# Optimization experiments

Hardware: AMD Instinct MI355X
Metric: run time of the kernel (lower is better)

The kernel has to match this reference:

```python
import jax, jax.numpy as jnp
import numpy as np

FP8_MAX = 448.0  # max representable magnitude of float8_e4m3fn


def _quantize_tensorwise(x):
    """Tensor-wise fp8 quantization. Returns (fp8 tensor, inverse_scale) where
    dequant = fp8.astype(f32) * inverse_scale (matches Fp8Quantization.quantize_tensorwise)."""
    amax = jnp.max(jnp.abs(x))
    inv_scale = jnp.maximum(amax / FP8_MAX, jnp.float32(1e-12))
    q = (x / inv_scale).astype(jnp.float8_e4m3fn)
    return q, inv_scale


def _fp8_mm(qa, qb, sa, sb):
    # scaled fp8 GEMM: accumulate in f32, apply product of per-tensor inverse scales
    return (qa.astype(jnp.float32) @ qb.astype(jnp.float32)) * (sa * sb)


def setup_inputs() -> dict:
    key = jax.random.key(0)
    k1, k2, k3 = jax.random.split(key, 3)
    x = jax.random.normal(k1, (4, 2048, 2048), dtype=jnp.float32)
    weight = jax.random.normal(k2, (2048, 2048), dtype=jnp.float32) * 0.02
    bias = jax.random.normal(k3, (2048,), dtype=jnp.float32) * 0.01
    return {"x": x, "weight": weight, "bias": bias}


def reference(x, weight, bias):
    # flatten leading dims: inputmat = input.view(-1, K)
    K = x.shape[-1]
    xm = x.reshape(-1, K)                      # [T, K]
    qx, sx = _quantize_tensorwise(xm)          # fp8 input + inverse scale
    qwt, swt = _quantize_tensorwise(weight.T)  # fp8 weight^T [K, N] + inverse scale
    out = _fp8_mm(qx, qwt, sx, swt) + bias     # [T, N]
    return out.reshape(*x.shape[:-1], -1)
```

## Files before the change

### kernel.cpp

```cpp
#include <hip/hip_runtime.h>
#include <stdint.h>

typedef float f32x4 __attribute__((ext_vector_type(4)));
typedef int   i32x4 __attribute__((ext_vector_type(4)));
typedef int   i32x8 __attribute__((ext_vector_type(8)));

__global__ __launch_bounds__(256) void amax2_kernel(
    const float* __restrict__ x, int nx4,
    const float* __restrict__ w, int nw4,
    int xblocks, int* __restrict__ out) {
  const float4* src;
  int n4, j0, stride, slot;
  if ((int)blockIdx.x < xblocks) {
    src = (const float4*)x; n4 = nx4; slot = 0;
    j0 = blockIdx.x * blockDim.x + threadIdx.x;
    stride = xblocks * blockDim.x;
  } else {
    src = (const float4*)w; n4 = nw4; slot = 1;
    j0 = (blockIdx.x - xblocks) * blockDim.x + threadIdx.x;
    stride = (gridDim.x - xblocks) * blockDim.x;
  }
  float m = 0.f;
  for (int j = j0; j < n4; j += stride) {
    float4 v = src[j];
    m = fmaxf(m, fmaxf(fmaxf(fabsf(v.x), fabsf(v.y)),
                       fmaxf(fabsf(v.z), fabsf(v.w))));
  }
#pragma unroll
  for (int off = 32; off; off >>= 1)
    m = fmaxf(m, __shfl_down(m, off, 64));
  __shared__ float red[4];
  const int lane = threadIdx.x & 63;
  const int wv = threadIdx.x >> 6;
  if (lane == 0) red[wv] = m;
  __syncthreads();
  if (threadIdx.x == 0) {
    m = fmaxf(fmaxf(red[0], red[1]), fmaxf(red[2], red[3]));
    atomicMax(out + slot, (int)__float_as_uint(m));
  }
}

__global__ __launch_bounds__(256) void quant2_kernel(
    const float* __restrict__ x, unsigned char* __restrict__ qx, int nx4,
    const float* __restrict__ w, unsigned char* __restrict__ qw, int nw4,
    int xblocks, const unsigned* __restrict__ amax2) {
  const float4* src;
  unsigned* dst;
  int n4, j0, stride;
  float amax;
  if ((int)blockIdx.x < xblocks) {
    src = (const float4*)x; dst = (unsigned*)qx; n4 = nx4;
    amax = __uint_as_float(amax2[0]);
    j0 = blockIdx.x * blockDim.x + threadIdx.x;
    stride = xblocks * blockDim.x;
  } else {
    src = (const float4*)w; dst = (unsigned*)qw; n4 = nw4;
    amax = __uint_as_float(amax2[1]);
    j0 = (blockIdx.x - xblocks) * blockDim.x + threadIdx.x;
    stride = (gridDim.x - xblocks) * blockDim.x;
  }
  const float inv_scale = fmaxf(amax / 448.0f, 1e-12f);
  for (int j = j0; j < n4; j += stride) {
    float4 v = src[j];
    float a0 = v.x / inv_scale;
    float a1 = v.y / inv_scale;
    float a2 = v.z / inv_scale;
    float a3 = v.w / inv_scale;
    int p = 0;
    p = __builtin_amdgcn_cvt_pk_fp8_f32(a0, a1, p, false);
    p = __builtin_amdgcn_cvt_pk_fp8_f32(a2, a3, p, true);
    dst[j] = (unsigned)p;
  }
}

#define BM 256
#define BN 256
#define BK 128
#define GEMM_LDS_BYTES (4 * 32768)

__device__ __forceinline__ void load_lds16(const void* g, void* l) {
  __builtin_amdgcn_global_load_lds(
      (const __attribute__((address_space(1))) unsigned int*)g,
      (__attribute__((address_space(3))) unsigned int*)l, 16, 0, 0);
}

__global__ __launch_bounds__(512, 2) void gemm_fp8_kernel(
    const unsigned char* __restrict__ Aq,
    const unsigned char* __restrict__ Bq,
    const float* __restrict__ bias,
    const unsigned* __restrict__ amax2,
    float* __restrict__ out,
    int T, int N, int K) {
  extern __shared__ unsigned char smem[];
  unsigned char* sA = smem;
  unsigned char* sB = smem + 65536;

  const int tid  = threadIdx.x;
  const int lane = tid & 63;
  const int wave = tid >> 6;
  const int wm = (wave >> 2) * 128;
  const int wn = (wave & 3) * 64;

  int lin = (int)(blockIdx.y * gridDim.x + blockIdx.x);
  const int nwg = (int)(gridDim.x * gridDim.y);
  if ((nwg & 7) == 0) lin = (lin & 7) * (nwg >> 3) + (lin >> 3);
  const long m0 = (long)(lin / (int)gridDim.x) * BM;
  const long n0 = (long)(lin % (int)gridDim.x) * BN;

  const long Kl = (long)K;

  const int row_s = tid >> 3;
  const int scol  = ((tid & 7) ^ (row_s & 7)) << 4;
  const int t16   = tid << 4;

  const int lm = lane & 15;
  const int qh = lane >> 4;
  const int c0 = ((qh * 2)     ^ (lm & 7)) << 4;
  const int c1 = ((qh * 2 + 1) ^ (lm & 7)) << 4;

  auto STAGE_A = [&](int Ts) {
    const unsigned char* g = Aq + (m0 + row_s) * Kl + (long)Ts * BK + scol;
    unsigned char* l = sA + ((Ts & 1) << 15) + t16;
    load_lds16(g, l);
    load_lds16(g +  64 * Kl, l + 8192);
    load_lds16(g + 128 * Kl, l + 16384);
    load_lds16(g + 192 * Kl, l + 24576);
  };
  auto STAGE_B = [&](int Ts) {
    const unsigned char* g = Bq + (n0 + row_s) * Kl + (long)Ts * BK + scol;
    unsigned char* l = sB + ((Ts & 1) << 15) + t16;
    load_lds16(g, l);
    load_lds16(g +  64 * Kl, l + 8192);
    load_lds16(g + 128 * Kl, l + 16384);
    load_lds16(g + 192 * Kl, l + 24576);
  };
  auto LDA = [&](const unsigned char* base, int mt) {
    const unsigned char* p = base + (wm + mt * 16 + lm) * BK;
    i32x4 lo = *(const i32x4*)(p + c0);
    i32x4 hi = *(const i32x4*)(p + c1);
    return (i32x8){lo.x, lo.y, lo.z, lo.w, hi.x, hi.y, hi.z, hi.w};
  };
  auto LDB = [&](const unsigned char* base, int nt) {
    const unsigned char* p = base + (wn + nt * 16 + lm) * BK;
    i32x4 lo = *(const i32x4*)(p + c0);
    i32x4 hi = *(const i32x4*)(p + c1);
    return (i32x8){lo.x, lo.y, lo.z, lo.w, hi.x, hi.y, hi.z, hi.w};
  };

  f32x4 acc[8][4];
#pragma unroll
  for (int i = 0; i < 8; ++i)
#pragma unroll
    for (int j = 0; j < 4; ++j) acc[i][j] = (f32x4){0.f, 0.f, 0.f, 0.f};

  const int nt = K / BK;

  STAGE_A(0); STAGE_B(0);
  asm volatile("s_waitcnt vmcnt(0)" ::: "memory");
  __builtin_amdgcn_s_barrier();
  __builtin_amdgcn_sched_barrier(0);

#define MFMA(ai, bj, ci)                                                 \
  acc[ci][bj] = __builtin_amdgcn_mfma_scale_f32_16x16x128_f8f6f4(        \
      af[ai], bf[bj], acc[ci][bj], 0, 0, 0, 0x7f7f7f7f, 0, 0x7f7f7f7f)

  i32x8 af[4], bf[4];
  for (int t = 0; t < nt; ++t) {
    const unsigned char* a = sA + ((t & 1) << 15);
    const unsigned char* b = sB + ((t & 1) << 15);

    if (t + 1 < nt) { STAGE_A(t + 1); STAGE_B(t + 1); }

    af[0] = LDA(a, 0); af[1] = LDA(a, 1); af[2] = LDA(a, 2); af[3] = LDA(a, 3);
    bf[0] = LDB(b, 0); bf[1] = LDB(b, 1); bf[2] = LDB(b, 2); bf[3] = LDB(b, 3);
#pragma unroll
    for (int i = 0; i < 4; ++i) {
      MFMA(i, 0, i); MFMA(i, 1, i); MFMA(i, 2, i); MFMA(i, 3, i);
    }

    __builtin_amdgcn_sched_barrier(0);

    af[0] = LDA(a, 4); af[1] = LDA(a, 5); af[2] = LDA(a, 6); af[3] = LDA(a, 7);
#pragma unroll
    for (int i = 0; i < 4; ++i) {
      MFMA(i, 0, 4 + i); MFMA(i, 1, 4 + i); MFMA(i, 2, 4 + i); MFMA(i, 3, 4 + i);
    }

    asm volatile("s_waitcnt vmcnt(0)" ::: "memory");
    __builtin_amdgcn_s_barrier();
    __builtin_amdgcn_sched_barrier(0);
  }
#undef MFMA

  const float fsx = fmaxf(__uint_as_float(amax2[0]) / 448.0f, 1e-12f);
  const float fsw = fmaxf(__uint_as_float(amax2[1]) / 448.0f, 1e-12f);
  const float scale = fsx * fsw;
  const int rbase = qh * 4;
  float bv[4];
#pragma unroll
  for (int j = 0; j < 4; ++j) bv[j] = bias[n0 + wn + j * 16 + lm];
#pragma unroll
  for (int mt = 0; mt < 8; ++mt) {
#pragma unroll
    for (int r = 0; r < 4; ++r) {
      const long row = m0 + wm + mt * 16 + rbase + r;
      float* orow = out + row * (long)N + n0 + wn;
#pragma unroll
      for (int j = 0; j < 4; ++j)
        orow[j * 16 + lm] = acc[mt][j][r] * scale + bv[j];
    }
  }
}

extern "C" void kernel_launch(void* const* d_in, const int* in_sizes, int n_in,
                              void* d_out, int out_size, void* d_ws, size_t ws_size,
                              hipStream_t stream) {
  const float* x = (const float*)d_in[0];
  const float* w = (const float*)d_in[1];
  const float* bias = (const float*)d_in[2];
  float* out = (float*)d_out;

  const int N = in_sizes[2];
  const int K = in_sizes[1] / N;
  const int T = in_sizes[0] / K;

  unsigned* amax2 = (unsigned*)d_ws;
  unsigned char* qx = (unsigned char*)d_ws + 256;
  unsigned char* qw = qx + (size_t)T * K;

  const int XB = 1024;
  const int WB = 256;
  amax2_kernel<<<XB + WB, 256, 0, stream>>>(x, T * K / 4, w, N * K / 4, XB,
                                            (int*)amax2);
  quant2_kernel<<<XB + WB, 256, 0, stream>>>(x, qx, T * K / 4, w, qw, N * K / 4,
                                             XB, amax2);

  static bool lds_attr_set = false;
  if (!lds_attr_set) {
    (void)hipFuncSetAttribute((const void*)gemm_fp8_kernel,
                              hipFuncAttributeMaxDynamicSharedMemorySize,
                              GEMM_LDS_BYTES);
    lds_attr_set = true;
  }
  dim3 grid(N / BN, T / BM);
  gemm_fp8_kernel<<<grid, 512, GEMM_LDS_BYTES, stream>>>(qx, qw, bias, amax2,
                                                         out, T, N, K);
}
```

Before: 178.7 us.

## Use 4 waves with 128x128 warp tiles in fp8 GEMM

The GEMM workgroup shrinks from 8 waves to 4, and each wave now computes a 128x128 output tile (8x8 MFMA tiles) instead of 128x64. Each thread issues twice as many global-to-LDS loads per stage, and all A and B fragments are loaded before one 64-MFMA block. The aim is more register-level reuse per LDS read and fewer waves contending for LDS. The cost is 256 accumulator registers per thread plus fragments, which risks spills or low occupancy, and less overlap between LDS reads and MFMAs.

```diff
diff --git a/kernel.cpp b/kernel.cpp
--- a/kernel.cpp
+++ b/kernel.cpp
@@ -84,7 +84,7 @@
       (__attribute__((address_space(3))) unsigned int*)l, 16, 0, 0);
 }
 
-__global__ __launch_bounds__(512, 2) void gemm_fp8_kernel(
+__global__ __launch_bounds__(256, 1) void gemm_fp8_kernel(
     const unsigned char* __restrict__ Aq,
     const unsigned char* __restrict__ Bq,
     const float* __restrict__ bias,
@@ -98,8 +98,8 @@
   const int tid  = threadIdx.x;
   const int lane = tid & 63;
   const int wave = tid >> 6;
-  const int wm = (wave >> 2) * 128;
-  const int wn = (wave & 3) * 64;
+  const int wm = (wave >> 1) * 128;
+  const int wn = (wave & 1) * 128;
 
   int lin = (int)(blockIdx.y * gridDim.x + blockIdx.x);
   const int nwg = (int)(gridDim.x * gridDim.y);
@@ -121,18 +121,16 @@
   auto STAGE_A = [&](int Ts) {
     const unsigned char* g = Aq + (m0 + row_s) * Kl + (long)Ts * BK + scol;
     unsigned char* l = sA + ((Ts & 1) << 15) + t16;
-    load_lds16(g, l);
-    load_lds16(g +  64 * Kl, l + 8192);
-    load_lds16(g + 128 * Kl, l + 16384);
-    load_lds16(g + 192 * Kl, l + 24576);
+#pragma unroll
+    for (int r = 0; r < 8; ++r)
+      load_lds16(g + (long)(r * 32) * Kl, l + r * 4096);
   };
   auto STAGE_B = [&](int Ts) {
     const unsigned char* g = Bq + (n0 + row_s) * Kl + (long)Ts * BK + scol;
     unsigned char* l = sB + ((Ts & 1) << 15) + t16;
-    load_lds16(g, l);
-    load_lds16(g +  64 * Kl, l + 8192);
-    load_lds16(g + 128 * Kl, l + 16384);
-    load_lds16(g + 192 * Kl, l + 24576);
+#pragma unroll
+    for (int r = 0; r < 8; ++r)
+      load_lds16(g + (long)(r * 32) * Kl, l + r * 4096);
   };
   auto LDA = [&](const unsigned char* base, int mt) {
     const unsigned char* p = base + (wm + mt * 16 + lm) * BK;
@@ -147,11 +145,11 @@
     return (i32x8){lo.x, lo.y, lo.z, lo.w, hi.x, hi.y, hi.z, hi.w};
   };
 
-  f32x4 acc[8][4];
+  f32x4 acc[8][8];
 #pragma unroll
   for (int i = 0; i < 8; ++i)
 #pragma unroll
-    for (int j = 0; j < 4; ++j) acc[i][j] = (f32x4){0.f, 0.f, 0.f, 0.f};
+    for (int j = 0; j < 8; ++j) acc[i][j] = (f32x4){0.f, 0.f, 0.f, 0.f};
 
   const int nt = K / BK;
 
@@ -160,45 +158,39 @@
   __builtin_amdgcn_s_barrier();
   __builtin_amdgcn_sched_barrier(0);
 
-#define MFMA(ai, bj, ci)                                                 \
-  acc[ci][bj] = __builtin_amdgcn_mfma_scale_f32_16x16x128_f8f6f4(        \
-      af[ai], bf[bj], acc[ci][bj], 0, 0, 0, 0x7f7f7f7f, 0, 0x7f7f7f7f)
-
-  i32x8 af[4], bf[4];
+  i32x8 af[8], bf[8];
   for (int t = 0; t < nt; ++t) {
     const unsigned char* a = sA + ((t & 1) << 15);
     const unsigned char* b = sB + ((t & 1) << 15);
 
     if (t + 1 < nt) { STAGE_A(t + 1); STAGE_B(t + 1); }
-
-    af[0] = LDA(a, 0); af[1] = LDA(a, 1); af[2] = LDA(a, 2); af[3] = LDA(a, 3);
-    bf[0] = LDB(b, 0); bf[1] = LDB(b, 1); bf[2] = LDB(b, 2); bf[3] = LDB(b, 3);
-#pragma unroll
-    for (int i = 0; i < 4; ++i) {
-      MFMA(i, 0, i); MFMA(i, 1, i); MFMA(i, 2, i); MFMA(i, 3, i);
-    }
-
     __builtin_amdgcn_sched_barrier(0);
 
-    af[0] = LDA(a, 4); af[1] = LDA(a, 5); af[2] = LDA(a, 6); af[3] = LDA(a, 7);
-#pragma unroll
-    for (int i = 0; i < 4; ++i) {
-      MFMA(i, 0, 4 + i); MFMA(i, 1, 4 + i); MFMA(i, 2, 4 + i); MFMA(i, 3, 4 + i);
-    }
+    af[0] = LDA(a, 0);
+#pragma unroll
+    for (int j = 0; j < 8; ++j) bf[j] = LDB(b, j);
+#pragma unroll
+    for (int i = 1; i < 8; ++i) af[i] = LDA(a, i);
+
+#pragma unroll
+    for (int i = 0; i < 8; ++i)
+#pragma unroll
+      for (int j = 0; j < 8; ++j)
+        acc[i][j] = __builtin_amdgcn_mfma_scale_f32_16x16x128_f8f6f4(
+            af[i], bf[j], acc[i][j], 0, 0, 0, 0x7f7f7f7f, 0, 0x7f7f7f7f);
 
     asm volatile("s_waitcnt vmcnt(0)" ::: "memory");
     __builtin_amdgcn_s_barrier();
     __builtin_amdgcn_sched_barrier(0);
   }
-#undef MFMA
 
   const float fsx = fmaxf(__uint_as_float(amax2[0]) / 448.0f, 1e-12f);
   const float fsw = fmaxf(__uint_as_float(amax2[1]) / 448.0f, 1e-12f);
   const float scale = fsx * fsw;
   const int rbase = qh * 4;
-  float bv[4];
-#pragma unroll
-  for (int j = 0; j < 4; ++j) bv[j] = bias[n0 + wn + j * 16 + lm];
+  float bv[8];
+#pragma unroll
+  for (int j = 0; j < 8; ++j) bv[j] = bias[n0 + wn + j * 16 + lm];
 #pragma unroll
   for (int mt = 0; mt < 8; ++mt) {
 #pragma unroll
@@ -206,7 +198,7 @@
       const long row = m0 + wm + mt * 16 + rbase + r;
       float* orow = out + row * (long)N + n0 + wn;
 #pragma unroll
-      for (int j = 0; j < 4; ++j)
+      for (int j = 0; j < 8; ++j)
         orow[j * 16 + lm] = acc[mt][j][r] * scale + bv[j];
     }
   }
@@ -243,6 +235,6 @@
     lds_attr_set = true;
   }
   dim3 grid(N / BN, T / BM);
-  gemm_fp8_kernel<<<grid, 512, GEMM_LDS_BYTES, stream>>>(qx, qw, bias, amax2,
+  gemm_fp8_kernel<<<grid, 256, GEMM_LDS_BYTES, stream>>>(qx, qw, bias, amax2,
                                                          out, T, N, K);
 }
```

Measured after the change: 187.2 us. 4.8% more time.

## Switch GEMM inner loop from 16x16x128 to 32x32x64 scaled fp8 MFMA

Applied to the files above, without the earlier changes.

Replaces the 16x16x128 MFMA tiling with 32x32x64 MFMA instructions. Each wave now computes a 128x64 tile as 4x2 blocks of 32x32, splitting BK=128 into two k-halves. The LDS fragment addressing, swizzle offsets and epilogue row mapping are reworked to match the 32x32 output layout. The larger MFMA shape needs fewer LDS fragment reads per FLOP, since each operand is reused across more outputs, but per-instruction latency rises and the accumulator registers are grouped differently.

```diff
diff --git a/kernel.cpp b/kernel.cpp
--- a/kernel.cpp
+++ b/kernel.cpp
@@ -1,9 +1,10 @@
 #include <hip/hip_runtime.h>
 #include <stdint.h>
 
-typedef float f32x4 __attribute__((ext_vector_type(4)));
-typedef int   i32x4 __attribute__((ext_vector_type(4)));
-typedef int   i32x8 __attribute__((ext_vector_type(8)));
+typedef float f32x4  __attribute__((ext_vector_type(4)));
+typedef float f32x16 __attribute__((ext_vector_type(16)));
+typedef int   i32x4  __attribute__((ext_vector_type(4)));
+typedef int   i32x8  __attribute__((ext_vector_type(8)));
 
 __global__ __launch_bounds__(256) void amax2_kernel(
     const float* __restrict__ x, int nx4,
@@ -113,10 +114,13 @@
   const int scol  = ((tid & 7) ^ (row_s & 7)) << 4;
   const int t16   = tid << 4;
 
-  const int lm = lane & 15;
-  const int qh = lane >> 4;
-  const int c0 = ((qh * 2)     ^ (lm & 7)) << 4;
-  const int c1 = ((qh * 2 + 1) ^ (lm & 7)) << 4;
+  const int lm = lane & 31;
+  const int qh = lane >> 5;
+  const int sw = lm & 7;
+  const int k0c0 = ((qh * 2)     ^ sw) << 4;
+  const int k0c1 = ((qh * 2 + 1) ^ sw) << 4;
+  const int k1c0 = ((4 + qh * 2)     ^ sw) << 4;
+  const int k1c1 = ((4 + qh * 2 + 1) ^ sw) << 4;
 
   auto STAGE_A = [&](int Ts) {
     const unsigned char* g = Aq + (m0 + row_s) * Kl + (long)Ts * BK + scol;
@@ -134,24 +138,17 @@
     load_lds16(g + 128 * Kl, l + 16384);
     load_lds16(g + 192 * Kl, l + 24576);
   };
-  auto LDA = [&](const unsigned char* base, int mt) {
-    const unsigned char* p = base + (wm + mt * 16 + lm) * BK;
-    i32x4 lo = *(const i32x4*)(p + c0);
-    i32x4 hi = *(const i32x4*)(p + c1);
-    return (i32x8){lo.x, lo.y, lo.z, lo.w, hi.x, hi.y, hi.z, hi.w};
+  auto LD = [&](const unsigned char* p, int ca, int cb) {
+    i32x4 lo = *(const i32x4*)(p + ca);
+    i32x4 hi = *(const i32x4*)(p + cb);
+    return __builtin_shufflevector(lo, hi, 0, 1, 2, 3, 4, 5, 6, 7);
   };
-  auto LDB = [&](const unsigned char* base, int nt) {
-    const unsigned char* p = base + (wn + nt * 16 + lm) * BK;
-    i32x4 lo = *(const i32x4*)(p + c0);
-    i32x4 hi = *(const i32x4*)(p + c1);
-    return (i32x8){lo.x, lo.y, lo.z, lo.w, hi.x, hi.y, hi.z, hi.w};
-  };
-
-  f32x4 acc[8][4];
-#pragma unroll
-  for (int i = 0; i < 8; ++i)
-#pragma unroll
-    for (int j = 0; j < 4; ++j) acc[i][j] = (f32x4){0.f, 0.f, 0.f, 0.f};
+
+  f32x16 acc[4][2];
+#pragma unroll
+  for (int i = 0; i < 4; ++i)
+#pragma unroll
+    for (int j = 0; j < 2; ++j) acc[i][j] = (f32x16)(0.f);
 
   const int nt = K / BK;
 
@@ -160,54 +157,65 @@
   __builtin_amdgcn_s_barrier();
   __builtin_amdgcn_sched_barrier(0);
 
-#define MFMA(ai, bj, ci)                                                 \
-  acc[ci][bj] = __builtin_amdgcn_mfma_scale_f32_16x16x128_f8f6f4(        \
-      af[ai], bf[bj], acc[ci][bj], 0, 0, 0, 0x7f7f7f7f, 0, 0x7f7f7f7f)
-
-  i32x8 af[4], bf[4];
+#define MM32(AF, BF, MT, NT)                                             \
+  acc[MT][NT] = __builtin_amdgcn_mfma_scale_f32_32x32x64_f8f6f4(         \
+      AF, BF, acc[MT][NT], 0, 0, 0, 0x7f7f7f7f, 0, 0x7f7f7f7f)
+
   for (int t = 0; t < nt; ++t) {
     const unsigned char* a = sA + ((t & 1) << 15);
     const unsigned char* b = sB + ((t & 1) << 15);
 
     if (t + 1 < nt) { STAGE_A(t + 1); STAGE_B(t + 1); }
 
-    af[0] = LDA(a, 0); af[1] = LDA(a, 1); af[2] = LDA(a, 2); af[3] = LDA(a, 3);
-    bf[0] = LDB(b, 0); bf[1] = LDB(b, 1); bf[2] = LDB(b, 2); bf[3] = LDB(b, 3);
-#pragma unroll
-    for (int i = 0; i < 4; ++i) {
-      MFMA(i, 0, i); MFMA(i, 1, i); MFMA(i, 2, i); MFMA(i, 3, i);
+    {
+      i32x8 bf0 = LD(b + (wn +  0 + lm) * BK, k0c0, k0c1);
+      i32x8 bf1 = LD(b + (wn + 32 + lm) * BK, k0c0, k0c1);
+      i32x8 af0 = LD(a + (wm +  0 + lm) * BK, k0c0, k0c1);
+      i32x8 af1 = LD(a + (wm + 32 + lm) * BK, k0c0, k0c1);
+      i32x8 af2 = LD(a + (wm + 64 + lm) * BK, k0c0, k0c1);
+      i32x8 af3 = LD(a + (wm + 96 + lm) * BK, k0c0, k0c1);
+      MM32(af0, bf0, 0, 0); MM32(af0, bf1, 0, 1);
+      MM32(af1, bf0, 1, 0); MM32(af1, bf1, 1, 1);
+      MM32(af2, bf0, 2, 0); MM32(af2, bf1, 2, 1);
+      MM32(af3, bf0, 3, 0); MM32(af3, bf1, 3, 1);
     }
 
     __builtin_amdgcn_sched_barrier(0);
 
-    af[0] = LDA(a, 4); af[1] = LDA(a, 5); af[2] = LDA(a, 6); af[3] = LDA(a, 7);
-#pragma unroll
-    for (int i = 0; i < 4; ++i) {
-      MFMA(i, 0, 4 + i); MFMA(i, 1, 4 + i); MFMA(i, 2, 4 + i); MFMA(i, 3, 4 + i);
+    {
+      i32x8 bf0 = LD(b + (wn +  0 + lm) * BK, k1c0, k1c1);
+      i32x8 bf1 = LD(b + (wn + 32 + lm) * BK, k1c0, k1c1);
+      i32x8 af0 = LD(a + (wm +  0 + lm) * BK, k1c0, k1c1);
+      i32x8 af1 = LD(a + (wm + 32 + lm) * BK, k1c0, k1c1);
+      i32x8 af2 = LD(a + (wm + 64 + lm) * BK, k1c0, k1c1);
+      i32x8 af3 = LD(a + (wm + 96 + lm) * BK, k1c0, k1c1);
+      MM32(af0, bf0, 0, 0); MM32(af0, bf1, 0, 1);
+      MM32(af1, bf0, 1, 0); MM32(af1, bf1, 1, 1);
+      MM32(af2, bf0, 2, 0); MM32(af2, bf1, 2, 1);
+      MM32(af3, bf0, 3, 0); MM32(af3, bf1, 3, 1);
     }
 
     asm volatile("s_waitcnt vmcnt(0)" ::: "memory");
     __builtin_amdgcn_s_barrier();
     __builtin_amdgcn_sched_barrier(0);
   }
-#undef MFMA
+#undef MM32
 
   const float fsx = fmaxf(__uint_as_float(amax2[0]) / 448.0f, 1e-12f);
   const float fsw = fmaxf(__uint_as_float(amax2[1]) / 448.0f, 1e-12f);
   const float scale = fsx * fsw;
-  const int rbase = qh * 4;
-  float bv[4];
-#pragma unroll
-  for (int j = 0; j < 4; ++j) bv[j] = bias[n0 + wn + j * 16 + lm];
-#pragma unroll
-  for (int mt = 0; mt < 8; ++mt) {
-#pragma unroll
-    for (int r = 0; r < 4; ++r) {
-      const long row = m0 + wm + mt * 16 + rbase + r;
+  float bv[2];
+#pragma unroll
+  for (int j = 0; j < 2; ++j) bv[j] = bias[n0 + wn + j * 32 + lm];
+#pragma unroll
+  for (int mt = 0; mt < 4; ++mt) {
+#pragma unroll
+    for (int r = 0; r < 16; ++r) {
+      const long row = m0 + wm + mt * 32 + (r & 3) + 8 * (r >> 2) + 4 * qh;
       float* orow = out + row * (long)N + n0 + wn;
 #pragma unroll
-      for (int j = 0; j < 4; ++j)
-        orow[j * 16 + lm] = acc[mt][j][r] * scale + bv[j];
+      for (int j = 0; j < 2; ++j)
+        orow[j * 32 + lm] = acc[mt][j][r] * scale + bv[j];
     }
   }
 }
```

Result: no change. 181.5 us (+1.6%).
